# Performance work log

Hardware: AMD Instinct MI355X
Metric: run time of the kernel (lower is better)

Reference implementation:

```python
import jax, jax.numpy as jnp
import numpy as np

T, B, I, H = 4096, 1, 1024, 1024

def setup_inputs() -> dict:
    key = jax.random.key(0)
    ks = jax.random.split(key, 8)
    s_i = 1.0 / np.sqrt(H)  # torch LSTM init scale
    x = jax.random.normal(ks[0], (T, B, I), dtype=jnp.float32)
    h0 = jnp.zeros((1, B, H), dtype=jnp.float32)
    c0 = jnp.zeros((1, B, H), dtype=jnp.float32)
    w_ih = jax.random.uniform(ks[1], (4 * H, I), jnp.float32, -s_i, s_i)
    w_hh = jax.random.uniform(ks[2], (4 * H, H), jnp.float32, -s_i, s_i)
    b_ih = jax.random.uniform(ks[3], (4 * H,), jnp.float32, -s_i, s_i)
    b_hh = jax.random.uniform(ks[4], (4 * H,), jnp.float32, -s_i, s_i)
    w_out = jax.random.uniform(ks[5], (1, H), jnp.float32, -s_i, s_i)
    b_out = jax.random.uniform(ks[6], (1,), jnp.float32, -s_i, s_i)
    return {"x": x, "h0": h0, "c0": c0, "w_ih": w_ih, "w_hh": w_hh,
            "b_ih": b_ih, "b_hh": b_hh, "w_out": w_out, "b_out": b_out}

def _lstm_scan(x, h0, c0, w_ih, w_hh, b_ih, b_hh):
    # Gate order i, f, g, o (PyTorch convention).
    b = b_ih + b_hh
    # Precompute input projections for all timesteps: [T, B, 4H]
    xg = jnp.einsum('tbi,gi->tbg', x, w_ih) + b

    def step(carry, xg_t):
        h, c = carry  # [B, H]
        gates = xg_t + h @ w_hh.T  # [B, 4H]
        i, f, g, o = jnp.split(gates, 4, axis=-1)
        i = jax.nn.sigmoid(i)
        f = jax.nn.sigmoid(f)
        g = jnp.tanh(g)
        o = jax.nn.sigmoid(o)
        c = f * c + i * g
        h = o * jnp.tanh(c)
        return (h, c), h

    (h, c), ys = jax.lax.scan(step, (h0[0], c0[0]), xg)
    return ys, h, c  # ys: [T, B, H]

def reference(x, h0, c0, w_ih, w_hh, b_ih, b_hh, w_out, b_out):
    ys, h, c = _lstm_scan(x, h0, c0, w_ih, w_hh, b_ih, b_hh)
    # train_once: output = tanh(linear_out(last LSTM output)), viewed (1, -1)
    pred = jnp.tanh(ys[-1] @ w_out.T + b_out)  # [B, 1]
    return pred
```

## Files before the change

### kernel.cpp

```cpp
#include <hip/hip_runtime.h>
#include <math.h>

#define T_STEPS 4096
#define HID     1024
#define G4      4096
#define NB      64

__device__ __forceinline__ unsigned long long ld64(const unsigned long long* p) {
    return __hip_atomic_load(p, __ATOMIC_RELAXED, __HIP_MEMORY_SCOPE_AGENT);
}
__device__ __forceinline__ void st64(unsigned long long* p, unsigned long long v) {
    __hip_atomic_store(p, v, __ATOMIC_RELAXED, __HIP_MEMORY_SCOPE_AGENT);
}
__device__ __forceinline__ unsigned long long packhv(float h, unsigned tag) {
    return ((unsigned long long)tag << 32) | (unsigned long long)__float_as_uint(h);
}

__global__ __launch_bounds__(256) void xg_gemm(
    const float* __restrict__ x, const float* __restrict__ w_ih,
    const float* __restrict__ b_ih, const float* __restrict__ b_hh,
    float* __restrict__ xg, unsigned long long* __restrict__ h_pub)
{
    if (blockIdx.x == 0 && blockIdx.y < 8)
        h_pub[blockIdx.y * 256 + threadIdx.x] = 0ull;

    __shared__ float Xs[32][68];
    __shared__ float Ws[32][68];

    const int t0  = blockIdx.y * 64;
    const int n0  = blockIdx.x * 64;
    const int thr = threadIdx.x;
    const int tx  = thr & 15;
    const int ty  = thr >> 4;

    float acc[4][4] = {};

    for (int kk = 0; kk < 1024; kk += 32) {
        #pragma unroll
        for (int i = 0; i < 2; i++) {
            int flat = thr + i * 256;
            int m    = flat >> 3;
            int kc   = flat & 7;
            float4 xv = *(const float4*)(x    + (size_t)(t0 + m) * 1024 + kk + kc * 4);
            float4 wv = *(const float4*)(w_ih + (size_t)(n0 + m) * 1024 + kk + kc * 4);
            Xs[kc*4+0][m] = xv.x; Xs[kc*4+1][m] = xv.y;
            Xs[kc*4+2][m] = xv.z; Xs[kc*4+3][m] = xv.w;
            Ws[kc*4+0][m] = wv.x; Ws[kc*4+1][m] = wv.y;
            Ws[kc*4+2][m] = wv.z; Ws[kc*4+3][m] = wv.w;
        }
        __syncthreads();
        #pragma unroll
        for (int k = 0; k < 32; k++) {
            float4 a4 = *(const float4*)&Xs[k][ty * 4];
            float4 b4 = *(const float4*)&Ws[k][tx * 4];
            float av[4] = {a4.x, a4.y, a4.z, a4.w};
            float bv[4] = {b4.x, b4.y, b4.z, b4.w};
            #pragma unroll
            for (int i = 0; i < 4; i++)
                #pragma unroll
                for (int j = 0; j < 4; j++)
                    acc[i][j] = fmaf(av[i], bv[j], acc[i][j]);
        }
        __syncthreads();
    }

    float4 bi = *(const float4*)(b_ih + n0 + tx * 4);
    float4 bh = *(const float4*)(b_hh + n0 + tx * 4);
    float bb[4] = {bi.x + bh.x, bi.y + bh.y, bi.z + bh.z, bi.w + bh.w};
    #pragma unroll
    for (int i = 0; i < 4; i++) {
        float4 o;
        o.x = acc[i][0] + bb[0]; o.y = acc[i][1] + bb[1];
        o.z = acc[i][2] + bb[2]; o.w = acc[i][3] + bb[3];
        *(float4*)(xg + (size_t)(t0 + ty * 4 + i) * G4 + n0 + tx * 4) = o;
    }
}

__global__ __launch_bounds__(512, 2) void lstm_rec(
    const float* __restrict__ xg, const float* __restrict__ w_hh,
    const float* __restrict__ h0, const float* __restrict__ c0,
    const float* __restrict__ w_out, const float* __restrict__ b_out,
    unsigned long long* __restrict__ h_pub,
    float* __restrict__ out)
{
    __shared__ float h_lds[64 * 20];
    __shared__ float g_lds[64];

    const int thr = threadIdx.x;
    const int b   = blockIdx.x;
    const int rg  = thr >> 6;
    const int ec  = thr & 63;

    float4 w[8][4];
    #pragma unroll
    for (int rr = 0; rr < 8; rr++) {
        const int s = rg * 8 + rr;
        const float* wr = w_hh + (size_t)((s >> 4) * HID + b * 16 + (s & 15)) * HID + ec * 16;
        #pragma unroll
        for (int q = 0; q < 4; q++)
            w[rr][q] = *(const float4*)(wr + q * 4);
    }

    float c = 0.0f;
    if (thr < 16) {
        c = c0[b * 16 + thr];
        st64(&h_pub[0 * HID + b * 16 + thr], packhv(h0[b * 16 + thr], 1u));
    }

    const int u0 = 2 * thr;
    const int l0 = (u0 >> 4) * 20 + (u0 & 15);

    for (int t = 0; t < T_STEPS; t++) {
        const int p = t & 1;

        const int sx = rg * 8 + (ec & 7);
        float xgv = (ec < 8)
            ? xg[(size_t)t * G4 + (sx >> 4) * HID + b * 16 + (sx & 15)] : 0.0f;

        const unsigned tag = (unsigned)(t + 1);
        const unsigned long long* a0 = &h_pub[p * HID + u0];
        unsigned long long v0 = ld64(a0), v1 = ld64(a0 + 1);
        while (((unsigned)(v0 >> 32) != tag) | ((unsigned)(v1 >> 32) != tag)) {
            v0 = ld64(a0); v1 = ld64(a0 + 1);
        }
        h_lds[l0]     = __uint_as_float((unsigned)v0);
        h_lds[l0 + 1] = __uint_as_float((unsigned)v1);
        __syncthreads();

        float4 h4[4];
        #pragma unroll
        for (int q = 0; q < 4; q++)
            h4[q] = *(const float4*)&h_lds[ec * 20 + q * 4];

        float a[8];
        #pragma unroll
        for (int rr = 0; rr < 8; rr++) {
            float s0 = 0.f, s1 = 0.f, s2 = 0.f, s3 = 0.f;
            #pragma unroll
            for (int q = 0; q < 4; q++) {
                s0 = fmaf(w[rr][q].x, h4[q].x, s0);
                s1 = fmaf(w[rr][q].y, h4[q].y, s1);
                s2 = fmaf(w[rr][q].z, h4[q].z, s2);
                s3 = fmaf(w[rr][q].w, h4[q].w, s3);
            }
            a[rr] = (s0 + s1) + (s2 + s3);
        }

        const bool b0 = (ec & 1), b1 = (ec & 2), b2 = (ec & 4);
        float f[4];
        #pragma unroll
        for (int i = 0; i < 4; i++) {
            float send = b0 ? a[2*i] : a[2*i+1];
            float recv = __shfl_xor(send, 1, 64);
            f[i] = (b0 ? a[2*i+1] : a[2*i]) + recv;
        }
        float g2[2];
        #pragma unroll
        for (int i = 0; i < 2; i++) {
            float send = b1 ? f[2*i] : f[2*i+1];
            float recv = __shfl_xor(send, 2, 64);
            g2[i] = (b1 ? f[2*i+1] : f[2*i]) + recv;
        }
        float d;
        {
            float send = b2 ? g2[0] : g2[1];
            float recv = __shfl_xor(send, 4, 64);
            d = (b2 ? g2[1] : g2[0]) + recv;
        }
        d += __shfl_xor(d, 8, 64);
        d += __shfl_xor(d, 16, 64);
        d += __shfl_xor(d, 32, 64);

        if (ec < 8) g_lds[rg * 8 + ec] = d + xgv;
        __syncthreads();

        if (thr < 16) {
            float gi = g_lds[thr];
            float gf = g_lds[16 + thr];
            float gg = g_lds[32 + thr];
            float go = g_lds[48 + thr];
            float si = 1.0f / (1.0f + expf(-gi));
            float sf = 1.0f / (1.0f + expf(-gf));
            float tg = tanhf(gg);
            float so = 1.0f / (1.0f + expf(-go));
            c = sf * c + si * tg;
            float hn = so * tanhf(c);
            st64(&h_pub[(p ^ 1) * HID + b * 16 + thr], packhv(hn, (unsigned)(t + 2)));
        }
    }

    if (b == 0) {
        const unsigned tag = (unsigned)(T_STEPS + 1);
        const unsigned long long* a0 = &h_pub[0 * HID + u0];
        unsigned long long v0 = ld64(a0), v1 = ld64(a0 + 1);
        while (((unsigned)(v0 >> 32) != tag) | ((unsigned)(v1 >> 32) != tag)) {
            v0 = ld64(a0); v1 = ld64(a0 + 1);
        }
        float part = __uint_as_float((unsigned)v0) * w_out[u0]
                   + __uint_as_float((unsigned)v1) * w_out[u0 + 1];
        #pragma unroll
        for (int m = 1; m < 64; m <<= 1)
            part += __shfl_xor(part, m, 64);
        __syncthreads();
        if (ec == 0) g_lds[rg] = part;
        __syncthreads();
        if (thr == 0) {
            float s = 0.f;
            #pragma unroll
            for (int i = 0; i < 8; i++) s += g_lds[i];
            out[0] = tanhf(s + b_out[0]);
        }
    }
}

extern "C" void kernel_launch(void* const* d_in, const int* in_sizes, int n_in,
                              void* d_out, int out_size, void* d_ws, size_t ws_size,
                              hipStream_t stream) {
    const float* x     = (const float*)d_in[0];
    const float* h0    = (const float*)d_in[1];
    const float* c0    = (const float*)d_in[2];
    const float* w_ih  = (const float*)d_in[3];
    const float* w_hh  = (const float*)d_in[4];
    const float* b_ih  = (const float*)d_in[5];
    const float* b_hh  = (const float*)d_in[6];
    const float* w_out = (const float*)d_in[7];
    const float* b_out = (const float*)d_in[8];
    float* out = (float*)d_out;

    char* ws = (char*)d_ws;
    float*              xg    = (float*)ws;
    unsigned long long* h_pub = (unsigned long long*)(ws + (size_t)T_STEPS * G4 * 4);

    xg_gemm<<<dim3(64, 64), 256, 0, stream>>>(x, w_ih, b_ih, b_hh, xg, h_pub);
    lstm_rec<<<NB, 512, 0, stream>>>(xg, w_hh, h0, c0, w_out, b_out, h_pub, out);
}
```

Measured before the change: 8.751 ms.

## Remap gate rows per wave to drop second block barrier and use fast math

Reassigns the recurrent weight rows so that each wavefront owns all four gates (i, f, g, o) for two hidden units. The gate nonlinearity and cell update can then run inside the wave using lane shuffles, with no shared-memory gate buffer and no second __syncthreads per timestep. h_lds is double-buffered by step parity so the single remaining barrier suffices. Sigmoid and tanh switch to __expf/__fdividef approximations, and an asm constraint pins the weights in VGPRs, trading a little accuracy for a shorter per-step serial path.

```diff
diff --git a/kernel.cpp b/kernel.cpp
--- a/kernel.cpp
+++ b/kernel.cpp
@@ -14,6 +14,12 @@
 }
 __device__ __forceinline__ unsigned long long packhv(float h, unsigned tag) {
     return ((unsigned long long)tag << 32) | (unsigned long long)__float_as_uint(h);
+}
+__device__ __forceinline__ float fsigmoid(float x) {
+    return __fdividef(1.0f, 1.0f + __expf(-x));
+}
+__device__ __forceinline__ float ftanh(float x) {
+    return __fdividef(2.0f, 1.0f + __expf(-2.0f * x)) - 1.0f;
 }
 
 __global__ __launch_bounds__(256) void xg_gemm(
@@ -83,39 +89,53 @@
     unsigned long long* __restrict__ h_pub,
     float* __restrict__ out)
 {
-    __shared__ float h_lds[64 * 20];
-    __shared__ float g_lds[64];
+    __shared__ float h_lds[2][64 * 20];
+    __shared__ float red_lds[8];
 
     const int thr = threadIdx.x;
     const int b   = blockIdx.x;
     const int rg  = thr >> 6;
     const int ec  = thr & 63;
 
-    float4 w[8][4];
+    int grow[8];
+    #pragma unroll
+    for (int rr = 0; rr < 8; rr++)
+        grow[rr] = (rr & 3) * HID + b * 16 + 2 * rg + (rr >> 2);
+
+    float w[8][16];
     #pragma unroll
     for (int rr = 0; rr < 8; rr++) {
-        const int s = rg * 8 + rr;
-        const float* wr = w_hh + (size_t)((s >> 4) * HID + b * 16 + (s & 15)) * HID + ec * 16;
-        #pragma unroll
-        for (int q = 0; q < 4; q++)
-            w[rr][q] = *(const float4*)(wr + q * 4);
-    }
-
+        const float* wr = w_hh + (size_t)grow[rr] * HID + ec * 16;
+        #pragma unroll
+        for (int q = 0; q < 4; q++) {
+            float4 v = *(const float4*)(wr + q * 4);
+            w[rr][q*4+0] = v.x; w[rr][q*4+1] = v.y;
+            w[rr][q*4+2] = v.z; w[rr][q*4+3] = v.w;
+        }
+    }
+    #pragma unroll
+    for (int rr = 0; rr < 8; rr++)
+        asm volatile("" :
+            "+v"(w[rr][0]),  "+v"(w[rr][1]),  "+v"(w[rr][2]),  "+v"(w[rr][3]),
+            "+v"(w[rr][4]),  "+v"(w[rr][5]),  "+v"(w[rr][6]),  "+v"(w[rr][7]),
+            "+v"(w[rr][8]),  "+v"(w[rr][9]),  "+v"(w[rr][10]), "+v"(w[rr][11]),
+            "+v"(w[rr][12]), "+v"(w[rr][13]), "+v"(w[rr][14]), "+v"(w[rr][15]));
+
+    const int myunit = b * 16 + 2 * rg + (ec >> 2);
     float c = 0.0f;
-    if (thr < 16) {
-        c = c0[b * 16 + thr];
-        st64(&h_pub[0 * HID + b * 16 + thr], packhv(h0[b * 16 + thr], 1u));
+    if (ec == 0 || ec == 4) {
+        c = c0[myunit];
+        st64(&h_pub[0 * HID + myunit], packhv(h0[myunit], 1u));
     }
 
     const int u0 = 2 * thr;
     const int l0 = (u0 >> 4) * 20 + (u0 & 15);
+    const int xrow = grow[ec & 7];
 
     for (int t = 0; t < T_STEPS; t++) {
         const int p = t & 1;
 
-        const int sx = rg * 8 + (ec & 7);
-        float xgv = (ec < 8)
-            ? xg[(size_t)t * G4 + (sx >> 4) * HID + b * 16 + (sx & 15)] : 0.0f;
+        float xgv = xg[(size_t)t * G4 + xrow];
 
         const unsigned tag = (unsigned)(t + 1);
         const unsigned long long* a0 = &h_pub[p * HID + u0];
@@ -123,14 +143,18 @@
         while (((unsigned)(v0 >> 32) != tag) | ((unsigned)(v1 >> 32) != tag)) {
             v0 = ld64(a0); v1 = ld64(a0 + 1);
         }
-        h_lds[l0]     = __uint_as_float((unsigned)v0);
-        h_lds[l0 + 1] = __uint_as_float((unsigned)v1);
+        h_lds[p][l0]     = __uint_as_float((unsigned)v0);
+        h_lds[p][l0 + 1] = __uint_as_float((unsigned)v1);
         __syncthreads();
 
         float4 h4[4];
         #pragma unroll
         for (int q = 0; q < 4; q++)
-            h4[q] = *(const float4*)&h_lds[ec * 20 + q * 4];
+            h4[q] = *(const float4*)&h_lds[p][ec * 20 + q * 4];
+        float hx[16] = {h4[0].x,h4[0].y,h4[0].z,h4[0].w,
+                        h4[1].x,h4[1].y,h4[1].z,h4[1].w,
+                        h4[2].x,h4[2].y,h4[2].z,h4[2].w,
+                        h4[3].x,h4[3].y,h4[3].z,h4[3].w};
 
         float a[8];
         #pragma unroll
@@ -138,10 +162,10 @@
             float s0 = 0.f, s1 = 0.f, s2 = 0.f, s3 = 0.f;
             #pragma unroll
             for (int q = 0; q < 4; q++) {
-                s0 = fmaf(w[rr][q].x, h4[q].x, s0);
-                s1 = fmaf(w[rr][q].y, h4[q].y, s1);
-                s2 = fmaf(w[rr][q].z, h4[q].z, s2);
-                s3 = fmaf(w[rr][q].w, h4[q].w, s3);
+                s0 = fmaf(w[rr][q*4+0], hx[q*4+0], s0);
+                s1 = fmaf(w[rr][q*4+1], hx[q*4+1], s1);
+                s2 = fmaf(w[rr][q*4+2], hx[q*4+2], s2);
+                s3 = fmaf(w[rr][q*4+3], hx[q*4+3], s3);
             }
             a[rr] = (s0 + s1) + (s2 + s3);
         }
@@ -170,22 +194,20 @@
         d += __shfl_xor(d, 8, 64);
         d += __shfl_xor(d, 16, 64);
         d += __shfl_xor(d, 32, 64);
-
-        if (ec < 8) g_lds[rg * 8 + ec] = d + xgv;
-        __syncthreads();
-
-        if (thr < 16) {
-            float gi = g_lds[thr];
-            float gf = g_lds[16 + thr];
-            float gg = g_lds[32 + thr];
-            float go = g_lds[48 + thr];
-            float si = 1.0f / (1.0f + expf(-gi));
-            float sf = 1.0f / (1.0f + expf(-gf));
-            float tg = tanhf(gg);
-            float so = 1.0f / (1.0f + expf(-go));
+        d += xgv;
+
+        float v1g = __shfl_xor(d, 1, 64);
+        float v2g = __shfl_xor(d, 2, 64);
+        float v3g = __shfl_xor(d, 3, 64);
+
+        if (ec == 0 || ec == 4) {
+            float si = fsigmoid(d);
+            float sf = fsigmoid(v1g);
+            float tg = ftanh(v2g);
+            float so = fsigmoid(v3g);
             c = sf * c + si * tg;
-            float hn = so * tanhf(c);
-            st64(&h_pub[(p ^ 1) * HID + b * 16 + thr], packhv(hn, (unsigned)(t + 2)));
+            float hn = so * ftanh(c);
+            st64(&h_pub[(p ^ 1) * HID + myunit], packhv(hn, (unsigned)(t + 2)));
         }
     }
 
@@ -202,12 +224,12 @@
         for (int m = 1; m < 64; m <<= 1)
             part += __shfl_xor(part, m, 64);
         __syncthreads();
-        if (ec == 0) g_lds[rg] = part;
+        if (ec == 0) red_lds[rg] = part;
         __syncthreads();
         if (thr == 0) {
             float s = 0.f;
             #pragma unroll
-            for (int i = 0; i < 8; i++) s += g_lds[i];
+            for (int i = 0; i < 8; i++) s += red_lds[i];
             out[0] = tanhf(s + b_out[0]);
         }
     }
```

After: 12.89 ms. +47.3%, slower.

## Spread LSTM recurrence over 256 blocks with one hidden unit per wavefront

Applied to the files above, without the earlier changes.

The persistent recurrent kernel now runs 256 blocks of 256 threads instead of 64 blocks of 512. Each wavefront owns one hidden unit's four gate rows, so the cross-wave LDS gate exchange and its second __syncthreads are replaced by shuffles within the wave. The h buffer in LDS is double-buffered, the gate nonlinearities use fast exp/divide intrinsics, and a large LDS pad forces one block per CU. The aim is to cut per-step latency by spreading the weight work over more CUs and removing a barrier. In exchange, each step's grid-wide spin on h_pub now involves four times as many publishers and pollers, and the fast intrinsics lose some accuracy.

```diff
diff --git a/kernel.cpp b/kernel.cpp
--- a/kernel.cpp
+++ b/kernel.cpp
@@ -4,7 +4,8 @@
 #define T_STEPS 4096
 #define HID     1024
 #define G4      4096
-#define NB      64
+#define NB      256
+#define TPB     256
 
 __device__ __forceinline__ unsigned long long ld64(const unsigned long long* p) {
     return __hip_atomic_load(p, __ATOMIC_RELAXED, __HIP_MEMORY_SCOPE_AGENT);
@@ -14,6 +15,12 @@
 }
 __device__ __forceinline__ unsigned long long packhv(float h, unsigned tag) {
     return ((unsigned long long)tag << 32) | (unsigned long long)__float_as_uint(h);
+}
+__device__ __forceinline__ float fsigmoid(float x) {
+    return __fdividef(1.0f, 1.0f + __expf(-x));
+}
+__device__ __forceinline__ float ftanh(float x) {
+    return __fdividef(2.0f, 1.0f + __expf(-2.0f * x)) - 1.0f;
 }
 
 __global__ __launch_bounds__(256) void xg_gemm(
@@ -76,138 +83,140 @@
     }
 }
 
-__global__ __launch_bounds__(512, 2) void lstm_rec(
+__global__ __launch_bounds__(256, 1) void lstm_rec(
     const float* __restrict__ xg, const float* __restrict__ w_hh,
     const float* __restrict__ h0, const float* __restrict__ c0,
     const float* __restrict__ w_out, const float* __restrict__ b_out,
     unsigned long long* __restrict__ h_pub,
     float* __restrict__ out)
 {
-    __shared__ float h_lds[64 * 20];
-    __shared__ float g_lds[64];
+    __shared__ float h_lds[2][64 * 20];
+    __shared__ float red_lds[4];
+    __shared__ float lds_pad[18432];
 
     const int thr = threadIdx.x;
     const int b   = blockIdx.x;
     const int rg  = thr >> 6;
     const int ec  = thr & 63;
 
-    float4 w[8][4];
+    if (thr == 0) ((volatile float*)lds_pad)[0] = 0.0f;
+
+    const int unit = 4 * b + rg;
+
+    float4 w4[4][4];
     #pragma unroll
-    for (int rr = 0; rr < 8; rr++) {
-        const int s = rg * 8 + rr;
-        const float* wr = w_hh + (size_t)((s >> 4) * HID + b * 16 + (s & 15)) * HID + ec * 16;
+    for (int rr = 0; rr < 4; rr++) {
+        const float* wr = w_hh + (size_t)(rr * HID + unit) * HID + ec * 16;
         #pragma unroll
         for (int q = 0; q < 4; q++)
-            w[rr][q] = *(const float4*)(wr + q * 4);
+            w4[rr][q] = *(const float4*)(wr + q * 4);
     }
 
     float c = 0.0f;
-    if (thr < 16) {
-        c = c0[b * 16 + thr];
-        st64(&h_pub[0 * HID + b * 16 + thr], packhv(h0[b * 16 + thr], 1u));
-    }
-
-    const int u0 = 2 * thr;
+    if (ec == 0) {
+        c = c0[unit];
+        st64(&h_pub[0 * HID + unit], packhv(h0[unit], 1u));
+    }
+
+    const int u0 = 4 * thr;
     const int l0 = (u0 >> 4) * 20 + (u0 & 15);
+    const int xrow = (ec & 3) * HID + unit;
 
     for (int t = 0; t < T_STEPS; t++) {
         const int p = t & 1;
 
-        const int sx = rg * 8 + (ec & 7);
-        float xgv = (ec < 8)
-            ? xg[(size_t)t * G4 + (sx >> 4) * HID + b * 16 + (sx & 15)] : 0.0f;
+        float xgv = xg[(size_t)t * G4 + xrow];
 
         const unsigned tag = (unsigned)(t + 1);
         const unsigned long long* a0 = &h_pub[p * HID + u0];
-        unsigned long long v0 = ld64(a0), v1 = ld64(a0 + 1);
-        while (((unsigned)(v0 >> 32) != tag) | ((unsigned)(v1 >> 32) != tag)) {
-            v0 = ld64(a0); v1 = ld64(a0 + 1);
-        }
-        h_lds[l0]     = __uint_as_float((unsigned)v0);
-        h_lds[l0 + 1] = __uint_as_float((unsigned)v1);
+        unsigned long long v0 = ld64(a0),     v1 = ld64(a0 + 1),
+                           v2 = ld64(a0 + 2), v3 = ld64(a0 + 3);
+        while (((unsigned)(v0 >> 32) != tag) | ((unsigned)(v1 >> 32) != tag) |
+               ((unsigned)(v2 >> 32) != tag) | ((unsigned)(v3 >> 32) != tag)) {
+            v0 = ld64(a0);     v1 = ld64(a0 + 1);
+            v2 = ld64(a0 + 2); v3 = ld64(a0 + 3);
+        }
+        float4 hw;
+        hw.x = __uint_as_float((unsigned)v0);
+        hw.y = __uint_as_float((unsigned)v1);
+        hw.z = __uint_as_float((unsigned)v2);
+        hw.w = __uint_as_float((unsigned)v3);
+        *(float4*)&h_lds[p][l0] = hw;
         __syncthreads();
 
         float4 h4[4];
         #pragma unroll
         for (int q = 0; q < 4; q++)
-            h4[q] = *(const float4*)&h_lds[ec * 20 + q * 4];
-
-        float a[8];
-        #pragma unroll
-        for (int rr = 0; rr < 8; rr++) {
+            h4[q] = *(const float4*)&h_lds[p][ec * 20 + q * 4];
+
+        float a[4];
+        #pragma unroll
+        for (int rr = 0; rr < 4; rr++) {
             float s0 = 0.f, s1 = 0.f, s2 = 0.f, s3 = 0.f;
             #pragma unroll
             for (int q = 0; q < 4; q++) {
-                s0 = fmaf(w[rr][q].x, h4[q].x, s0);
-                s1 = fmaf(w[rr][q].y, h4[q].y, s1);
-                s2 = fmaf(w[rr][q].z, h4[q].z, s2);
-                s3 = fmaf(w[rr][q].w, h4[q].w, s3);
+                s0 = fmaf(w4[rr][q].x, h4[q].x, s0);
+                s1 = fmaf(w4[rr][q].y, h4[q].y, s1);
+                s2 = fmaf(w4[rr][q].z, h4[q].z, s2);
+                s3 = fmaf(w4[rr][q].w, h4[q].w, s3);
             }
             a[rr] = (s0 + s1) + (s2 + s3);
         }
 
-        const bool b0 = (ec & 1), b1 = (ec & 2), b2 = (ec & 4);
-        float f[4];
-        #pragma unroll
-        for (int i = 0; i < 4; i++) {
+        const bool b0 = (ec & 1), b1 = (ec & 2);
+        float f[2];
+        #pragma unroll
+        for (int i = 0; i < 2; i++) {
             float send = b0 ? a[2*i] : a[2*i+1];
             float recv = __shfl_xor(send, 1, 64);
             f[i] = (b0 ? a[2*i+1] : a[2*i]) + recv;
         }
-        float g2[2];
-        #pragma unroll
-        for (int i = 0; i < 2; i++) {
-            float send = b1 ? f[2*i] : f[2*i+1];
-            float recv = __shfl_xor(send, 2, 64);
-            g2[i] = (b1 ? f[2*i+1] : f[2*i]) + recv;
-        }
         float d;
         {
-            float send = b2 ? g2[0] : g2[1];
-            float recv = __shfl_xor(send, 4, 64);
-            d = (b2 ? g2[1] : g2[0]) + recv;
-        }
+            float send = b1 ? f[0] : f[1];
+            float recv = __shfl_xor(send, 2, 64);
+            d = (b1 ? f[1] : f[0]) + recv;
+        }
+        d += __shfl_xor(d, 4, 64);
         d += __shfl_xor(d, 8, 64);
         d += __shfl_xor(d, 16, 64);
         d += __shfl_xor(d, 32, 64);
-
-        if (ec < 8) g_lds[rg * 8 + ec] = d + xgv;
-        __syncthreads();
-
-        if (thr < 16) {
-            float gi = g_lds[thr];
-            float gf = g_lds[16 + thr];
-            float gg = g_lds[32 + thr];
-            float go = g_lds[48 + thr];
-            float si = 1.0f / (1.0f + expf(-gi));
-            float sf = 1.0f / (1.0f + expf(-gf));
-            float tg = tanhf(gg);
-            float so = 1.0f / (1.0f + expf(-go));
-            c = sf * c + si * tg;
-            float hn = so * tanhf(c);
-            st64(&h_pub[(p ^ 1) * HID + b * 16 + thr], packhv(hn, (unsigned)(t + 2)));
+        d += xgv;
+
+        float nl = ((ec & 3) == 2) ? ftanh(d) : fsigmoid(d);
+        float sf = __shfl_xor(nl, 1, 64);
+        float tg = __shfl_xor(nl, 2, 64);
+        float so = __shfl_xor(nl, 3, 64);
+
+        if (ec == 0) {
+            c = sf * c + nl * tg;
+            float hn = so * ftanh(c);
+            st64(&h_pub[(p ^ 1) * HID + unit], packhv(hn, (unsigned)(t + 2)));
         }
     }
 
     if (b == 0) {
         const unsigned tag = (unsigned)(T_STEPS + 1);
         const unsigned long long* a0 = &h_pub[0 * HID + u0];
-        unsigned long long v0 = ld64(a0), v1 = ld64(a0 + 1);
-        while (((unsigned)(v0 >> 32) != tag) | ((unsigned)(v1 >> 32) != tag)) {
-            v0 = ld64(a0); v1 = ld64(a0 + 1);
+        unsigned long long v0 = ld64(a0),     v1 = ld64(a0 + 1),
+                           v2 = ld64(a0 + 2), v3 = ld64(a0 + 3);
+        while (((unsigned)(v0 >> 32) != tag) | ((unsigned)(v1 >> 32) != tag) |
+               ((unsigned)(v2 >> 32) != tag) | ((unsigned)(v3 >> 32) != tag)) {
+            v0 = ld64(a0);     v1 = ld64(a0 + 1);
+            v2 = ld64(a0 + 2); v3 = ld64(a0 + 3);
         }
         float part = __uint_as_float((unsigned)v0) * w_out[u0]
-                   + __uint_as_float((unsigned)v1) * w_out[u0 + 1];
+                   + __uint_as_float((unsigned)v1) * w_out[u0 + 1]
+                   + __uint_as_float((unsigned)v2) * w_out[u0 + 2]
+                   + __uint_as_float((unsigned)v3) * w_out[u0 + 3];
         #pragma unroll
         for (int m = 1; m < 64; m <<= 1)
             part += __shfl_xor(part, m, 64);
         __syncthreads();
-        if (ec == 0) g_lds[rg] = part;
+        if (ec == 0) red_lds[rg] = part;
         __syncthreads();
         if (thr == 0) {
-            float s = 0.f;
-            #pragma unroll
-            for (int i = 0; i < 8; i++) s += g_lds[i];
+            float s = red_lds[0] + red_lds[1] + red_lds[2] + red_lds[3];
             out[0] = tanhf(s + b_out[0]);
         }
     }
@@ -232,5 +241,5 @@
     unsigned long long* h_pub = (unsigned long long*)(ws + (size_t)T_STEPS * G4 * 4);
 
     xg_gemm<<<dim3(64, 64), 256, 0, stream>>>(x, w_ih, b_ih, b_hh, xg, h_pub);
-    lstm_rec<<<NB, 512, 0, stream>>>(xg, w_hh, h0, c0, w_out, b_out, h_pub, out);
-}
+    lstm_rec<<<NB, TPB, 0, stream>>>(xg, w_hh, h0, c0, w_out, b_out, h_pub, out);
+}
```

Result: slower. 17.49 ms (+99.9%).
